# Kernel optimization log

Measured on AMD Instinct MI355X. Metric: run time of the kernel, lower is better.

The kernel has to match this reference:

```python
import jax, jax.numpy as jnp
import numpy as np


def _bn(x, g, b):
    # per-feature batch norm over (batch, seq), training-style statistics
    mu = jnp.mean(x, axis=(0, 1), keepdims=True)
    var = jnp.var(x, axis=(0, 1), keepdims=True)
    return (x - mu) * jax.lax.rsqrt(var + 1e-5) * g + b


def _heads(x, H):
    B, S, D = x.shape
    return x.reshape(B, S, H, D // H).transpose(0, 2, 1, 3)  # [B,H,S,hd]


def _merge(x):
    B, H, S, hd = x.shape
    return x.transpose(0, 2, 1, 3).reshape(B, S, H * hd)


def _pos_encoding(S, D, dtype):
    p = jnp.arange(S, dtype=jnp.float32)[:, None]
    i = jnp.arange(D // 2, dtype=jnp.float32)[None, :]
    ang = p / jnp.power(10000.0, 2.0 * i / D)
    # interleave sin (even dims) and cos (odd dims)
    return jnp.stack([jnp.sin(ang), jnp.cos(ang)], axis=-1).reshape(S, D).astype(dtype)


def _forward(x, encod, embed, Wq, bq, Wk, bk, Wv, bv, g1, b1,
             Wq2, bq2, Wk2, bk2, Wv2, bv2, Wo2, bo2, g2, b2, Wf, bf,
             num_heads, N):
    D = embed.shape[1]
    emb = embed[x]                      # [B,S,D]
    S = emb.shape[1]
    # forward does embed + (embed + pos) == 2*embed + pos
    input_multi = 2.0 * emb + _pos_encoding(S, D, emb.dtype)
    scale1 = 1.0 / np.sqrt(D)           # original scales by sqrt(embed_dim)
    scale2 = 1.0 / np.sqrt(D // num_heads)
    for _ in range(N):
        q, k, v = jnp.split(input_multi, 3, axis=-1)   # each [B,S,D/3]
        Q = _heads(jax.nn.relu(q @ Wq + bq), num_heads)
        K = _heads(jax.nn.relu(k @ Wk + bk), num_heads)
        Vm = _heads(jax.nn.relu(v @ Wv + bv), num_heads)
        A = jax.nn.softmax(jnp.einsum('bhqd,bhkd->bhqk', Q, K) * scale1, axis=-1)
        sa = _merge(jnp.einsum('bhqk,bhkd->bhqd', A, Vm))
        t = _bn(input_multi + sa, g1, b1)
        # cross attention: q,k from encoder halves, v from decoder state
        eq, ek = jnp.split(encod, 2, axis=-1)          # each [B,S,D/2]
        Q2 = _heads(eq @ Wq2 + bq2, num_heads)
        K2 = _heads(ek @ Wk2 + bk2, num_heads)
        V2 = _heads(t @ Wv2 + bv2, num_heads)
        A2 = jax.nn.softmax(jnp.einsum('bhqd,bhkd->bhqk', Q2, K2) * scale2, axis=-1)
        m2 = _merge(jnp.einsum('bhqk,bhkd->bhqd', A2, V2)) @ Wo2 + bo2
        t = _bn(m2 + t, g2, b2)
        # add_norm_2 reused for the FFN residual, as in the source
        input_multi = _bn(t + (t @ Wf + bf), g2, b2)
    return input_multi


def setup_inputs() -> dict:
    B, S, D, H, V, N = 4, 1024, 768, 12, 32000, 2
    ks = jax.random.split(jax.random.key(0), 12)
    w = lambda k, shape: jax.random.normal(k, shape, jnp.float32) * 0.02
    zeros = lambda: jnp.zeros((D,), jnp.float32)
    ones = lambda: jnp.ones((D,), jnp.float32)
    return {
        'x': jax.random.randint(ks[0], (B, S), 0, V),
        'encod': jax.random.normal(ks[1], (B, S, D), jnp.float32),
        'embed': w(ks[2], (V, D)),
        'Wq': w(ks[3], (D // 3, D)), 'bq': zeros(),
        'Wk': w(ks[4], (D // 3, D)), 'bk': zeros(),
        'Wv': w(ks[5], (D // 3, D)), 'bv': zeros(),
        'g1': ones(), 'b1': zeros(),
        'Wq2': w(ks[6], (D // 2, D)), 'bq2': zeros(),
        'Wk2': w(ks[7], (D // 2, D)), 'bk2': zeros(),
        'Wv2': w(ks[8], (D, D)), 'bv2': zeros(),
        'Wo2': w(ks[9], (D, D)), 'bo2': zeros(),
        'g2': ones(), 'b2': zeros(),
        'Wf': w(ks[10], (D, D)), 'bf': zeros(),
        'num_heads': H, 'N': N,
    }


def reference(x, encod, embed, Wq, bq, Wk, bk, Wv, bv, g1, b1,
              Wq2, bq2, Wk2, bk2, Wv2, bv2, Wo2, bo2, g2, b2, Wf, bf,
              num_heads, N):
    return _forward(x, encod, embed, Wq, bq, Wk, bk, Wv, bv, g1, b1,
                    Wq2, bq2, Wk2, bk2, Wv2, bv2, Wo2, bo2, g2, b2, Wf, bf,
                    num_heads, N)
```

## Files before the change

kernel.cpp:

```cpp
#include <hip/hip_runtime.h>
#include <hip/hip_bf16.h>

#define B 4
#define S 1024
#define D 768
#define H 12
#define HD 64
#define MROWS (B * S)
#define NELEM (B * S * D)

typedef __attribute__((ext_vector_type(8))) short short8;
typedef __attribute__((ext_vector_type(4))) short s16x4;
typedef __attribute__((ext_vector_type(4))) float f32x4;

#define MFMA16(a, b, c) __builtin_amdgcn_mfma_f32_16x16x32_bf16(a, b, c, 0, 0, 0)

#define SWZ64(row, col)  ((col) ^ (((row) & 7) << 3))
#define SWZ128(row, col) ((col) ^ (((row) & 15) << 3))

static __device__ __forceinline__ float bs2f(short s) {
    unsigned int u = ((unsigned int)(unsigned short)s) << 16;
    float f;
    __builtin_memcpy(&f, &u, 4);
    return f;
}
static __device__ __forceinline__ short f2bs(float f) {
    __hip_bfloat16 h = __float2bfloat16(f);
    return __builtin_bit_cast(short, h);
}
static __device__ __forceinline__ float loadin(const void* p, size_t i, int isb) {
    return isb ? bs2f(((const short*)p)[i]) : ((const float*)p)[i];
}

__global__ void detect_k(const void* p, int* flag) {
    const short* hb = (const short*)p;
    int t = threadIdx.x;
    int ins = 0;
    #pragma unroll
    for (int j = 0; j < 4; j++) {
        float v = bs2f(hb[(t * 4 + j) * 2]);
        if (!(v == v) || fabsf(v) > 1e3f || (v != 0.0f && fabsf(v) < 1e-20f)) ins++;
    }
    #pragma unroll
    for (int off = 32; off; off >>= 1) ins += __shfl_xor(ins, off);
    if (t == 0) *flag = (ins > 64) ? 0 : 1;
}

__global__ __launch_bounds__(256) void embed_pos_k(const int* __restrict__ x,
                                                   const void* __restrict__ embed,
                                                   float* __restrict__ outf,
                                                   short* __restrict__ outb,
                                                   const int* __restrict__ flg) {
    const int f = *flg;
    int bs = blockIdx.x;
    int tok = x[bs];
    int s = bs & (S - 1);
    for (int j = threadIdx.x; j < D; j += 256) {
        float e = loadin(embed, (size_t)tok * D + j, f);
        int i = j >> 1;
        float ang = (float)s * __expf(-9.210340371976184f * (2.0f * (float)i) / (float)D);
        float p = (j & 1) ? cosf(ang) : sinf(ang);
        float v = 2.0f * e + p;
        outf[bs * D + j] = v;
        outb[bs * D + j] = f2bs(v);
    }
}

struct WSegs {
    const void* src[8];
    short* dst[8];
    int K[8];
    const void* esrc;
    short* edst;
    float* statz;
};

__global__ __launch_bounds__(256) void prep_k(WSegs sg, const int* __restrict__ flg) {
    const int f = *flg;
    const int seg = blockIdx.z;
    const int t = threadIdx.x;
    if (seg == 8) {
        int tid = (blockIdx.y * 12 + blockIdx.x) * 256 + t;
        if (tid < 9216) sg.statz[tid] = 0.f;
        for (int i = tid; i < NELEM; i += 12 * 12 * 256)
            sg.edst[i] = f2bs(loadin(sg.esrc, i, f));
        return;
    }
    const int K = sg.K[seg];
    const int k0 = blockIdx.y * 64;
    if (k0 >= K) return;
    const void* src = sg.src[seg];
    short* dst = sg.dst[seg];
    __shared__ __align__(16) short Ts[64 * 72];
    int n0 = blockIdx.x * 64;
    int r = t >> 2, c4 = (t & 3) * 16;
    #pragma unroll
    for (int j = 0; j < 16; j++)
        Ts[r * 72 + c4 + j] = f2bs(loadin(src, (size_t)(k0 + r) * D + n0 + c4 + j, f));
    __syncthreads();
    int n = t >> 2, kc = (t & 3) * 16;
    short tmp[16];
    #pragma unroll
    for (int j = 0; j < 16; j++) tmp[j] = Ts[(kc + j) * 72 + n];
    short* dchunk = dst + (size_t)(n0 + n) * K + k0 + kc;
    *(short8*)&dchunk[0] = *(const short8*)&tmp[0];
    *(short8*)&dchunk[8] = *(const short8*)&tmp[8];
}

__global__ __launch_bounds__(256) void store_norm_k(const float* __restrict__ a,
                                                    const float* __restrict__ sums,
                                                    const void* __restrict__ g,
                                                    const void* __restrict__ beta,
                                                    void* __restrict__ out,
                                                    const int* __restrict__ flg) {
    const int f = *flg;
    int i = blockIdx.x * 256 + threadIdx.x;
    if (i < NELEM) {
        int ft = i % D;
        float mean = sums[ft] * (1.0f / (float)MROWS);
        float var = sums[D + ft] * (1.0f / (float)MROWS) - mean * mean;
        float sc = rsqrtf(var + 1e-5f) * loadin(g, ft, f);
        float y = (a[i] - mean) * sc + loadin(beta, ft, f);
        if (f) ((short*)out)[i] = f2bs(y);
        else   ((float*)out)[i] = y;
    }
}

struct GJob {
    const void* A;
    const short* WT;
    const void* bias;
    void* out;
    const float* resid;
    const float* bnsums;
    const void* bng;
    const void* bnb;
    float* sacc;
    int K;
    int aoff;
    int relu;
    int mode;
    int anorm;
    int rnorm;
};
struct GJobs { GJob j[3]; };

__global__ __launch_bounds__(256) void mgemm_k(GJobs js, const int* __restrict__ flg) {
    const GJob J = js.j[blockIdx.z];
    const int f = *flg;
    __shared__ __align__(16) short As[2][64 * 64];
    __shared__ __align__(16) short Bs[2][64 * 64];
    __shared__ float ssb0[768];
    __shared__ float ssb1[768];
    const int t = threadIdx.x;
    const int wave = t >> 6, lane = t & 63;
    const int quad = lane >> 4, l16 = lane & 15;
    if (J.anorm) {
        for (int i = t; i < D; i += 256) {
            float mean = J.bnsums[i] * (1.0f / (float)MROWS);
            float var = J.bnsums[D + i] * (1.0f / (float)MROWS) - mean * mean;
            float sc = rsqrtf(var + 1e-5f) * loadin(J.bng, i, f);
            ssb0[i] = sc;
            ssb1[i] = loadin(J.bnb, i, f) - mean * sc;
        }
        __syncthreads();
    }
    int lin = blockIdx.y * gridDim.x + blockIdx.x;
    int per = (gridDim.x * gridDim.y) >> 3;
    int nl = (lin & 7) * per + (lin >> 3);
    const int n0 = (nl % gridDim.x) * 64;
    const int m0 = (nl / gridDim.x) * 64;
    const int wm = (wave >> 1) * 32;
    const int wn = (wave & 1) * 32;
    f32x4 acc[2][2];
    #pragma unroll
    for (int i = 0; i < 2; i++)
        #pragma unroll
        for (int j = 0; j < 2; j++) acc[i][j] = f32x4{0.f, 0.f, 0.f, 0.f};

    const int ar = t >> 2;
    const int ac = (t & 3) * 16;
    const int wsz0 = SWZ64(ar, ac);
    const int wsz1 = SWZ64(ar, ac + 8);
    const int K = J.K;

    auto stageA = [&](int k0, short8& r0, short8& r1) {
        if (J.anorm) {
            int ft = J.aoff + k0 + ac;
            const float* Af = (const float*)J.A + (size_t)(m0 + ar) * 768 + ft;
            f32x4 v0 = *(const f32x4*)&Af[0];
            f32x4 v1 = *(const f32x4*)&Af[4];
            f32x4 v2 = *(const f32x4*)&Af[8];
            f32x4 v3 = *(const f32x4*)&Af[12];
            f32x4 c0 = *(const f32x4*)&ssb0[ft];
            f32x4 c1 = *(const f32x4*)&ssb0[ft + 4];
            f32x4 c2 = *(const f32x4*)&ssb0[ft + 8];
            f32x4 c3 = *(const f32x4*)&ssb0[ft + 12];
            f32x4 h0 = *(const f32x4*)&ssb1[ft];
            f32x4 h1 = *(const f32x4*)&ssb1[ft + 4];
            f32x4 h2 = *(const f32x4*)&ssb1[ft + 8];
            f32x4 h3 = *(const f32x4*)&ssb1[ft + 12];
            #pragma unroll
            for (int e = 0; e < 4; e++) {
                r0[e]     = f2bs(v0[e] * c0[e] + h0[e]);
                r0[4 + e] = f2bs(v1[e] * c1[e] + h1[e]);
                r1[e]     = f2bs(v2[e] * c2[e] + h2[e]);
                r1[4 + e] = f2bs(v3[e] * c3[e] + h3[e]);
            }
        } else {
            const short* Ab = (const short*)J.A + (size_t)(m0 + ar) * 768 + k0 + ac;
            r0 = *(const short8*)&Ab[0];
            r1 = *(const short8*)&Ab[8];
        }
    };

    {
        short8 a0, a1, b0, b1;
        stageA(0, a0, a1);
        const short* Wb = &J.WT[(size_t)(n0 + ar) * K + ac];
        b0 = *(const short8*)&Wb[0];
        b1 = *(const short8*)&Wb[8];
        *(short8*)&As[0][ar * 64 + wsz0] = a0;
        *(short8*)&As[0][ar * 64 + wsz1] = a1;
        *(short8*)&Bs[0][ar * 64 + wsz0] = b0;
        *(short8*)&Bs[0][ar * 64 + wsz1] = b1;
    }
    __syncthreads();

    int cur = 0;
    for (int k0 = 0; k0 < K; k0 += 64) {
        short8 na0, na1, nb0, nb1;
        const bool more = (k0 + 64 < K);
        if (more) {
            stageA(k0 + 64, na0, na1);
            const short* Wb = &J.WT[(size_t)(n0 + ar) * K + k0 + 64 + ac];
            nb0 = *(const short8*)&Wb[0];
            nb1 = *(const short8*)&Wb[8];
        }
        #pragma unroll
        for (int kk = 0; kk < 2; kk++) {
            short8 af[2], bfr[2];
            #pragma unroll
            for (int i = 0; i < 2; i++) {
                int arow = wm + i * 16 + l16;
                af[i] = *(const short8*)&As[cur][arow * 64 + SWZ64(arow, kk * 32 + quad * 8)];
            }
            #pragma unroll
            for (int j = 0; j < 2; j++) {
                int brow = wn + j * 16 + l16;
                bfr[j] = *(const short8*)&Bs[cur][brow * 64 + SWZ64(brow, kk * 32 + quad * 8)];
            }
            #pragma unroll
            for (int i = 0; i < 2; i++)
                #pragma unroll
                for (int j = 0; j < 2; j++)
                    acc[i][j] = MFMA16(af[i], bfr[j], acc[i][j]);
        }
        if (more) {
            *(short8*)&As[cur ^ 1][ar * 64 + wsz0] = na0;
            *(short8*)&As[cur ^ 1][ar * 64 + wsz1] = na1;
            *(short8*)&Bs[cur ^ 1][ar * 64 + wsz0] = nb0;
            *(short8*)&Bs[cur ^ 1][ar * 64 + wsz1] = nb1;
        }
        __syncthreads();
        cur ^= 1;
    }

    if (J.mode == 3) {
        short* sb = &As[0][0];
        #pragma unroll
        for (int j = 0; j < 2; j++) {
            int coll = wn + j * 16 + l16;
            float bv = loadin(J.bias, n0 + coll, f);
            #pragma unroll
            for (int i = 0; i < 2; i++) {
                int rowl = wm + i * 16 + quad * 4;
                s16x4 pk;
                #pragma unroll
                for (int r = 0; r < 4; r++) {
                    float v = acc[i][j][r] + bv;
                    if (J.relu) v = fmaxf(v, 0.f);
                    pk[r] = f2bs(v);
                }
                *(s16x4*)&sb[coll * 72 + rowl] = pk;
            }
        }
        __syncthreads();
        int hd = t >> 2, c = (t & 3) * 16;
        int b = m0 >> 10, s0 = m0 & (S - 1), h = n0 >> 6;
        short* dst = (short*)J.out + (((size_t)(b * H + h) * HD + hd) * S + s0 + c);
        *(short8*)&dst[0] = *(const short8*)&sb[hd * 72 + c];
        *(short8*)&dst[8] = *(const short8*)&sb[hd * 72 + c + 8];
    } else {
        #pragma unroll
        for (int j = 0; j < 2; j++) {
            int col = n0 + wn + j * 16 + l16;
            float bv = loadin(J.bias, col, f);
            float rsc = 1.f, rsh = 0.f;
            if (J.rnorm) {
                float mean = J.bnsums[col] * (1.0f / (float)MROWS);
                float var = J.bnsums[D + col] * (1.0f / (float)MROWS) - mean * mean;
                rsc = rsqrtf(var + 1e-5f) * loadin(J.bng, col, f);
                rsh = loadin(J.bnb, col, f) - mean * rsc;
            }
            float s1 = 0.f, s2 = 0.f;
            #pragma unroll
            for (int i = 0; i < 2; i++) {
                int rowb = m0 + wm + i * 16 + quad * 4;
                #pragma unroll
                for (int r = 0; r < 4; r++) {
                    float v = acc[i][j][r] + bv;
                    if (J.relu) v = fmaxf(v, 0.f);
                    int row = rowb + r;
                    if (J.mode == 2) {
                        size_t idx = (size_t)row * D + col;
                        if (J.resid) {
                            float rv = J.resid[idx];
                            v += J.rnorm ? (rv * rsc + rsh) : rv;
                        }
                        ((float*)J.out)[idx] = v;
                        s1 += v;
                        s2 += v * v;
                    } else if (J.mode == 1) {
                        size_t idx = (((size_t)(row >> 10) * H + (col >> 6)) * S + (row & (S - 1))) * HD + (col & 63);
                        ((short*)J.out)[idx] = f2bs(v);
                    } else {
                        ((short*)J.out)[(size_t)row * D + col] = f2bs(v);
                    }
                }
            }
            if (J.mode == 2 && J.sacc) {
                s1 += __shfl_xor(s1, 16); s1 += __shfl_xor(s1, 32);
                s2 += __shfl_xor(s2, 16); s2 += __shfl_xor(s2, 32);
                if (quad == 0) {
                    atomicAdd(&J.sacc[col], s1);
                    atomicAdd(&J.sacc[D + col], s2);
                }
            }
        }
    }
}

__global__ __launch_bounds__(256) void mfma_attn_fo_k(const short* __restrict__ Q,
                                                      const short* __restrict__ Km,
                                                      const short* __restrict__ Vt,
                                                      void* __restrict__ out,
                                                      const float* __restrict__ resid,
                                                      const float* __restrict__ rsums,
                                                      const void* __restrict__ rg,
                                                      const void* __restrict__ rb,
                                                      float* __restrict__ sacc,
                                                      float scale, int obf,
                                                      const int* __restrict__ flg) {
    __shared__ __align__(16) short Ks[128 * 64];
    __shared__ __align__(16) short Vs[64 * 128];
    __shared__ __align__(16) short Ps[4][16 * 136];
    const int fl = *flg;
    const int qt = blockIdx.y;
    const int bh = blockIdx.x;
    const int b = bh / H, h = bh % H;
    const int t = threadIdx.x;
    const int wave = t >> 6, lane = t & 63, quad = lane >> 4, l16 = lane & 15;
    const float sc2 = scale * 1.44269504089f;
    const short* Qh = Q + (size_t)bh * S * HD;
    const short* Kh = Km + (size_t)bh * S * HD;
    const short* Vh = Vt + (size_t)bh * S * HD;
    const int qrow = qt * 64 + wave * 16 + l16;
    short8 qf0 = *(const short8*)&Qh[(size_t)qrow * 64 + quad * 8];
    short8 qf1 = *(const short8*)&Qh[(size_t)qrow * 64 + 32 + quad * 8];
    short8 ones;
    #pragma unroll
    for (int j = 0; j < 8; j++) ones[j] = (short)0x3F80;
    f32x4 o[4];
    f32x4 ls = f32x4{0.f, 0.f, 0.f, 0.f};
    float m_i = -1e30f;
    #pragma unroll
    for (int nt = 0; nt < 4; nt++) o[nt] = f32x4{0.f, 0.f, 0.f, 0.f};
    const int krow = t >> 1, kc0 = (t & 1) * 32;
    const int vhd = t >> 2, vkc = (t & 3) * 32;
    const short* kbase = &Kh[(size_t)krow * 64 + kc0];
    const short* vbase = &Vh[(size_t)vhd * S + vkc];

    short8 kreg[4], vreg[4];
    #pragma unroll
    for (int j = 0; j < 4; j++) kreg[j] = *(const short8*)&kbase[j * 8];
    #pragma unroll
    for (int j = 0; j < 4; j++) vreg[j] = *(const short8*)&vbase[j * 8];
    #pragma unroll
    for (int j = 0; j < 4; j++)
        *(short8*)&Ks[krow * 64 + SWZ64(krow, kc0 + j * 8)] = kreg[j];
    #pragma unroll
    for (int j = 0; j < 4; j++)
        *(short8*)&Vs[vhd * 128 + SWZ128(vhd, vkc + j * 8)] = vreg[j];
    __syncthreads();

    for (int kt = 0; kt < S; kt += 128) {
        if (kt + 128 < S) {
            #pragma unroll
            for (int j = 0; j < 4; j++)
                kreg[j] = *(const short8*)&kbase[(size_t)(kt + 128) * 64 + j * 8];
            #pragma unroll
            for (int j = 0; j < 4; j++)
                vreg[j] = *(const short8*)&vbase[kt + 128 + j * 8];
        }
        f32x4 sf[8];
        #pragma unroll
        for (int nt = 0; nt < 8; nt++) {
            int kr = nt * 16 + l16;
            short8 kb0 = *(const short8*)&Ks[kr * 64 + SWZ64(kr, quad * 8)];
            short8 kb1 = *(const short8*)&Ks[kr * 64 + SWZ64(kr, 32 + quad * 8)];
            f32x4 c = f32x4{0.f, 0.f, 0.f, 0.f};
            c = MFMA16(kb0, qf0, c);
            c = MFMA16(kb1, qf1, c);
            sf[nt] = c;
        }
        f32x4 m4 = sf[0];
        #pragma unroll
        for (int nt = 1; nt < 8; nt++)
            #pragma unroll
            for (int r = 0; r < 4; r++) m4[r] = fmaxf(m4[r], sf[nt][r]);
        float mx = fmaxf(fmaxf(m4[0], m4[1]), fmaxf(m4[2], m4[3]));
        mx = fmaxf(mx, __shfl_xor(mx, 16));
        mx = fmaxf(mx, __shfl_xor(mx, 32));
        bool need = ((mx - m_i) * sc2 > 8.0f);
        if (__any(need)) {
            float mnew = fmaxf(m_i, mx);
            float alpha = exp2f((m_i - mnew) * sc2);
            m_i = mnew;
            #pragma unroll
            for (int r = 0; r < 4; r++) {
                float ar = __shfl(alpha, quad * 4 + r);
                ls[r] *= ar;
                #pragma unroll
                for (int nt = 0; nt < 4; nt++) o[nt][r] *= ar;
            }
        }
        #pragma unroll
        for (int nt = 0; nt < 8; nt++) {
            s16x4 pk;
            #pragma unroll
            for (int r = 0; r < 4; r++)
                pk[r] = f2bs(exp2f((sf[nt][r] - m_i) * sc2));
            *(s16x4*)&Ps[wave][l16 * 136 + nt * 16 + quad * 4] = pk;
        }
        short8 pa[4];
        #pragma unroll
        for (int kc = 0; kc < 4; kc++)
            pa[kc] = *(const short8*)&Ps[wave][l16 * 136 + kc * 32 + quad * 8];
        #pragma unroll
        for (int nt = 0; nt < 4; nt++) {
            int vr = nt * 16 + l16;
            #pragma unroll
            for (int kc = 0; kc < 4; kc++) {
                short8 vb = *(const short8*)&Vs[vr * 128 + SWZ128(vr, kc * 32 + quad * 8)];
                o[nt] = MFMA16(pa[kc], vb, o[nt]);
            }
        }
        #pragma unroll
        for (int kc = 0; kc < 4; kc++) ls = MFMA16(pa[kc], ones, ls);
        __syncthreads();
        if (kt + 128 < S) {
            #pragma unroll
            for (int j = 0; j < 4; j++)
                *(short8*)&Ks[krow * 64 + SWZ64(krow, kc0 + j * 8)] = kreg[j];
            #pragma unroll
            for (int j = 0; j < 4; j++)
                *(short8*)&Vs[vhd * 128 + SWZ128(vhd, vkc + j * 8)] = vreg[j];
        }
        __syncthreads();
    }
    float inv[4];
    #pragma unroll
    for (int r = 0; r < 4; r++) inv[r] = 1.0f / ls[r];
    #pragma unroll
    for (int nt = 0; nt < 4; nt++) {
        int col = h * HD + nt * 16 + l16;
        float rsc = 1.f, rsh = 0.f;
        if (rsums) {
            float mean = rsums[col] * (1.0f / (float)MROWS);
            float var = rsums[D + col] * (1.0f / (float)MROWS) - mean * mean;
            rsc = rsqrtf(var + 1e-5f) * loadin(rg, col, fl);
            rsh = loadin(rb, col, fl) - mean * rsc;
        }
        float s1 = 0.f, s2 = 0.f;
        #pragma unroll
        for (int r = 0; r < 4; r++) {
            int row = b * S + qt * 64 + wave * 16 + quad * 4 + r;
            size_t idx = (size_t)row * D + col;
            float v = o[nt][r] * inv[r];
            if (obf) {
                ((short*)out)[idx] = f2bs(v);
            } else {
                if (resid) {
                    float rv = resid[idx];
                    v += rsums ? (rv * rsc + rsh) : rv;
                }
                ((float*)out)[idx] = v;
                s1 += v;
                s2 += v * v;
            }
        }
        if (sacc) {
            s1 += __shfl_xor(s1, 16); s1 += __shfl_xor(s1, 32);
            s2 += __shfl_xor(s2, 16); s2 += __shfl_xor(s2, 32);
            if (quad == 0) {
                atomicAdd(&sacc[col], s1);
                atomicAdd(&sacc[D + col], s2);
            }
        }
    }
}

extern "C" void kernel_launch(void* const* d_in, const int* in_sizes, int n_in,
                              void* d_out, int out_size, void* d_ws, size_t ws_size,
                              hipStream_t stream) {
    const int* x = (const int*)d_in[0];
    const short* encod = (const short*)d_in[1];
    const short* embed = (const short*)d_in[2];
    const short* Wq = (const short*)d_in[3];
    const short* bq = (const short*)d_in[4];
    const short* Wk = (const short*)d_in[5];
    const short* bk = (const short*)d_in[6];
    const short* Wv = (const short*)d_in[7];
    const short* bv = (const short*)d_in[8];
    const short* g1 = (const short*)d_in[9];
    const short* b1 = (const short*)d_in[10];
    const short* Wq2 = (const short*)d_in[11];
    const short* bq2 = (const short*)d_in[12];
    const short* Wk2 = (const short*)d_in[13];
    const short* bk2 = (const short*)d_in[14];
    const short* Wv2 = (const short*)d_in[15];
    const short* bv2 = (const short*)d_in[16];
    const short* Wo2 = (const short*)d_in[17];
    const short* bo2 = (const short*)d_in[18];
    const short* g2 = (const short*)d_in[19];
    const short* b2 = (const short*)d_in[20];
    const short* Wf = (const short*)d_in[21];
    const short* bf_ = (const short*)d_in[22];

    short* HBase = (short*)d_ws;
    #define HB(i) (HBase + (size_t)(i) * NELEM)
    float* IMf = (float*)HB(0);
    short* IMb = HB(2);
    short* Q2h = HB(3);
    short* K2h = HB(4);
    short* WTp = HB(5);
    short* WTq  = WTp;
    short* WTk  = WTp + 196608;
    short* WTv  = WTp + 393216;
    short* WTq2 = WTp + 589824;
    short* WTk2 = WTp + 884736;
    short* WTv2 = WTp + 1179648;
    short* WTo2 = WTp + 1769472;
    short* WTf  = WTp + 2359296;
    short* Qbh = HB(6);
    short* Kbh = HB(7);
    short* Vth = HB(9);
    float* T1f = (float*)HB(10);
    float* Ff  = (float*)HB(12);
    short* A2b = HB(15);
    float* T2f = (float*)HB(16);
    short* Eb  = Qbh;
    float* SU = (float*)HB(18);
    #define SUMS(it, bn) (SU + (size_t)((it) * 3 + (bn)) * 2 * D)
    int*   flg  = (int*)(SU + 12 * D);

    const dim3 gGrid(12, 64);
    const dim3 aGrid(B * H, S / 64);
    const int EB = (NELEM + 255) / 256;
    const float scale1 = 0.03608439182435161f;
    const float scale2 = 0.125f;

    detect_k<<<1, 64, 0, stream>>>(encod, flg);
    embed_pos_k<<<MROWS, 256, 0, stream>>>(x, embed, IMf, IMb, flg);

    WSegs sg;
    sg.src[0] = Wq;  sg.dst[0] = WTq;  sg.K[0] = 256;
    sg.src[1] = Wk;  sg.dst[1] = WTk;  sg.K[1] = 256;
    sg.src[2] = Wv;  sg.dst[2] = WTv;  sg.K[2] = 256;
    sg.src[3] = Wq2; sg.dst[3] = WTq2; sg.K[3] = 384;
    sg.src[4] = Wk2; sg.dst[4] = WTk2; sg.K[4] = 384;
    sg.src[5] = Wv2; sg.dst[5] = WTv2; sg.K[5] = 768;
    sg.src[6] = Wo2; sg.dst[6] = WTo2; sg.K[6] = 768;
    sg.src[7] = Wf;  sg.dst[7] = WTf;  sg.K[7] = 768;
    sg.esrc = encod; sg.edst = Eb; sg.statz = SU;
    prep_k<<<dim3(12, 12, 9), 256, 0, stream>>>(sg, flg);

    {
        GJobs js;
        js.j[0] = GJob{Eb,       WTq2, bq2, Q2h, nullptr, nullptr, nullptr, nullptr, nullptr, 384, 0, 0, 1, 0, 0};
        js.j[1] = GJob{Eb + 384, WTk2, bk2, K2h, nullptr, nullptr, nullptr, nullptr, nullptr, 384, 0, 0, 1, 0, 0};
        js.j[2] = js.j[0];
        mgemm_k<<<dim3(12, 64, 2), 256, 0, stream>>>(js, flg);
    }

    for (int it = 0; it < 2; it++) {
        {
            GJobs js;
            if (it == 0) {
                js.j[0] = GJob{IMb,       WTq, bq, Qbh, nullptr, nullptr, nullptr, nullptr, nullptr, 256, 0,   1, 1, 0, 0};
                js.j[1] = GJob{IMb + 256, WTk, bk, Kbh, nullptr, nullptr, nullptr, nullptr, nullptr, 256, 0,   1, 1, 0, 0};
                js.j[2] = GJob{IMb + 512, WTv, bv, Vth, nullptr, nullptr, nullptr, nullptr, nullptr, 256, 0,   1, 3, 0, 0};
            } else {
                js.j[0] = GJob{Ff, WTq, bq, Qbh, nullptr, SUMS(0, 2), g2, b2, nullptr, 256, 0,   1, 1, 1, 0};
                js.j[1] = GJob{Ff, WTk, bk, Kbh, nullptr, SUMS(0, 2), g2, b2, nullptr, 256, 256, 1, 1, 1, 0};
                js.j[2] = GJob{Ff, WTv, bv, Vth, nullptr, SUMS(0, 2), g2, b2, nullptr, 256, 512, 1, 3, 1, 0};
            }
            mgemm_k<<<dim3(12, 64, 3), 256, 0, stream>>>(js, flg);
        }
        if (it == 0)
            mfma_attn_fo_k<<<aGrid, 256, 0, stream>>>(Qbh, Kbh, Vth, T1f, IMf,
                    nullptr, nullptr, nullptr, SUMS(0, 0), scale1, 0, flg);
        else
            mfma_attn_fo_k<<<aGrid, 256, 0, stream>>>(Qbh, Kbh, Vth, T1f, Ff,
                    SUMS(0, 2), g2, b2, SUMS(1, 0), scale1, 0, flg);
        {
            GJobs js;
            js.j[0] = GJob{T1f, WTv2, bv2, Vth, nullptr, SUMS(it, 0), g1, b1, nullptr, 768, 0, 0, 3, 1, 0};
            js.j[1] = js.j[0]; js.j[2] = js.j[0];
            mgemm_k<<<gGrid, 256, 0, stream>>>(js, flg);
        }
        mfma_attn_fo_k<<<aGrid, 256, 0, stream>>>(Q2h, K2h, Vth, A2b, nullptr,
                nullptr, nullptr, nullptr, nullptr, scale2, 1, flg);
        {
            GJobs js;
            js.j[0] = GJob{A2b, WTo2, bo2, T2f, T1f, SUMS(it, 0), g1, b1, SUMS(it, 1), 768, 0, 0, 2, 0, 1};
            js.j[1] = js.j[0]; js.j[2] = js.j[0];
            mgemm_k<<<gGrid, 256, 0, stream>>>(js, flg);
        }
        {
            GJobs js;
            js.j[0] = GJob{T2f, WTf, bf_, Ff, T2f, SUMS(it, 1), g2, b2, SUMS(it, 2), 768, 0, 0, 2, 1, 1};
            js.j[1] = js.j[0]; js.j[2] = js.j[0];
            mgemm_k<<<gGrid, 256, 0, stream>>>(js, flg);
        }
    }

    store_norm_k<<<EB, 256, 0, stream>>>(Ff, SUMS(1, 2), g2, b2, d_out, flg);
}
```

Baseline: 569.9 us.

## Template GEMM on K, prefetch two stages ahead, use packed bf16 conversion

The GEMM kernel is templated on K so its k-loop fully unrolls. Global loads are now issued two stages ahead using register double-buffering on top of the shared-memory ping-pong, which aims to hide more global latency. Scalar float-to-bf16 conversions in the GEMM A staging, the epilogue and the attention P tile are replaced with the packed v_cvt_pk_bf16_f32 instruction to cut VALU work. In exchange, register pressure rises from the extra prefetch buffers and the unrolled loop, and several template instantiations are compiled.

```diff
diff --git a/kernel.cpp b/kernel.cpp
--- a/kernel.cpp
+++ b/kernel.cpp
@@ -27,6 +27,11 @@
 static __device__ __forceinline__ short f2bs(float f) {
     __hip_bfloat16 h = __float2bfloat16(f);
     return __builtin_bit_cast(short, h);
+}
+static __device__ __forceinline__ unsigned int cvtpk_bf16(float lo, float hi) {
+    unsigned int r;
+    asm("v_cvt_pk_bf16_f32 %0, %1, %2" : "=v"(r) : "v"(lo), "v"(hi));
+    return r;
 }
 static __device__ __forceinline__ float loadin(const void* p, size_t i, int isb) {
     return isb ? bs2f(((const short*)p)[i]) : ((const float*)p)[i];
@@ -145,6 +150,7 @@
 };
 struct GJobs { GJob j[3]; };
 
+template<int KT>
 __global__ __launch_bounds__(256) void mgemm_k(GJobs js, const int* __restrict__ flg) {
     const GJob J = js.j[blockIdx.z];
     const int f = *flg;
@@ -182,7 +188,7 @@
     const int ac = (t & 3) * 16;
     const int wsz0 = SWZ64(ar, ac);
     const int wsz1 = SWZ64(ar, ac + 8);
-    const int K = J.K;
+    constexpr int NS = KT / 64;
 
     auto stageA = [&](int k0, short8& r0, short8& r1) {
         if (J.anorm) {
@@ -200,43 +206,51 @@
             f32x4 h1 = *(const f32x4*)&ssb1[ft + 4];
             f32x4 h2 = *(const f32x4*)&ssb1[ft + 8];
             f32x4 h3 = *(const f32x4*)&ssb1[ft + 12];
-            #pragma unroll
-            for (int e = 0; e < 4; e++) {
-                r0[e]     = f2bs(v0[e] * c0[e] + h0[e]);
-                r0[4 + e] = f2bs(v1[e] * c1[e] + h1[e]);
-                r1[e]     = f2bs(v2[e] * c2[e] + h2[e]);
-                r1[4 + e] = f2bs(v3[e] * c3[e] + h3[e]);
-            }
+            union { unsigned int u[4]; short8 s; } ca, cb;
+            ca.u[0] = cvtpk_bf16(v0[0] * c0[0] + h0[0], v0[1] * c0[1] + h0[1]);
+            ca.u[1] = cvtpk_bf16(v0[2] * c0[2] + h0[2], v0[3] * c0[3] + h0[3]);
+            ca.u[2] = cvtpk_bf16(v1[0] * c1[0] + h1[0], v1[1] * c1[1] + h1[1]);
+            ca.u[3] = cvtpk_bf16(v1[2] * c1[2] + h1[2], v1[3] * c1[3] + h1[3]);
+            cb.u[0] = cvtpk_bf16(v2[0] * c2[0] + h2[0], v2[1] * c2[1] + h2[1]);
+            cb.u[1] = cvtpk_bf16(v2[2] * c2[2] + h2[2], v2[3] * c2[3] + h2[3]);
+            cb.u[2] = cvtpk_bf16(v3[0] * c3[0] + h3[0], v3[1] * c3[1] + h3[1]);
+            cb.u[3] = cvtpk_bf16(v3[2] * c3[2] + h3[2], v3[3] * c3[3] + h3[3]);
+            r0 = ca.s;
+            r1 = cb.s;
         } else {
             const short* Ab = (const short*)J.A + (size_t)(m0 + ar) * 768 + k0 + ac;
             r0 = *(const short8*)&Ab[0];
             r1 = *(const short8*)&Ab[8];
         }
     };
+    auto loadB = [&](int k0, short8& r0, short8& r1) {
+        const short* Wb = &J.WT[(size_t)(n0 + ar) * KT + k0 + ac];
+        r0 = *(const short8*)&Wb[0];
+        r1 = *(const short8*)&Wb[8];
+    };
 
     {
         short8 a0, a1, b0, b1;
         stageA(0, a0, a1);
-        const short* Wb = &J.WT[(size_t)(n0 + ar) * K + ac];
-        b0 = *(const short8*)&Wb[0];
-        b1 = *(const short8*)&Wb[8];
+        loadB(0, b0, b1);
         *(short8*)&As[0][ar * 64 + wsz0] = a0;
         *(short8*)&As[0][ar * 64 + wsz1] = a1;
         *(short8*)&Bs[0][ar * 64 + wsz0] = b0;
         *(short8*)&Bs[0][ar * 64 + wsz1] = b1;
     }
+    short8 pA0, pA1, pB0, pB1;
+    stageA(64, pA0, pA1);
+    loadB(64, pB0, pB1);
     __syncthreads();
 
-    int cur = 0;
-    for (int k0 = 0; k0 < K; k0 += 64) {
-        short8 na0, na1, nb0, nb1;
-        const bool more = (k0 + 64 < K);
-        if (more) {
-            stageA(k0 + 64, na0, na1);
-            const short* Wb = &J.WT[(size_t)(n0 + ar) * K + k0 + 64 + ac];
-            nb0 = *(const short8*)&Wb[0];
-            nb1 = *(const short8*)&Wb[8];
-        }
+    #pragma unroll
+    for (int s = 0; s < NS; s++) {
+        short8 nA0, nA1, nB0, nB1;
+        if (s + 2 < NS) {
+            stageA((s + 2) * 64, nA0, nA1);
+            loadB((s + 2) * 64, nB0, nB1);
+        }
+        const int cur = s & 1;
         #pragma unroll
         for (int kk = 0; kk < 2; kk++) {
             short8 af[2], bfr[2];
@@ -256,14 +270,14 @@
                 for (int j = 0; j < 2; j++)
                     acc[i][j] = MFMA16(af[i], bfr[j], acc[i][j]);
         }
-        if (more) {
-            *(short8*)&As[cur ^ 1][ar * 64 + wsz0] = na0;
-            *(short8*)&As[cur ^ 1][ar * 64 + wsz1] = na1;
-            *(short8*)&Bs[cur ^ 1][ar * 64 + wsz0] = nb0;
-            *(short8*)&Bs[cur ^ 1][ar * 64 + wsz1] = nb1;
-        }
+        if (s + 1 < NS) {
+            *(short8*)&As[cur ^ 1][ar * 64 + wsz0] = pA0;
+            *(short8*)&As[cur ^ 1][ar * 64 + wsz1] = pA1;
+            *(short8*)&Bs[cur ^ 1][ar * 64 + wsz0] = pB0;
+            *(short8*)&Bs[cur ^ 1][ar * 64 + wsz1] = pB1;
+        }
+        pA0 = nA0; pA1 = nA1; pB0 = nB0; pB1 = nB1;
         __syncthreads();
-        cur ^= 1;
     }
 
     if (J.mode == 3) {
@@ -275,14 +289,16 @@
             #pragma unroll
             for (int i = 0; i < 2; i++) {
                 int rowl = wm + i * 16 + quad * 4;
-                s16x4 pk;
-                #pragma unroll
-                for (int r = 0; r < 4; r++) {
-                    float v = acc[i][j][r] + bv;
-                    if (J.relu) v = fmaxf(v, 0.f);
-                    pk[r] = f2bs(v);
+                float e0 = acc[i][j][0] + bv, e1 = acc[i][j][1] + bv;
+                float e2 = acc[i][j][2] + bv, e3 = acc[i][j][3] + bv;
+                if (J.relu) {
+                    e0 = fmaxf(e0, 0.f); e1 = fmaxf(e1, 0.f);
+                    e2 = fmaxf(e2, 0.f); e3 = fmaxf(e3, 0.f);
                 }
-                *(s16x4*)&sb[coll * 72 + rowl] = pk;
+                union { unsigned int u[2]; s16x4 s; } cv;
+                cv.u[0] = cvtpk_bf16(e0, e1);
+                cv.u[1] = cvtpk_bf16(e2, e3);
+                *(s16x4*)&sb[coll * 72 + rowl] = cv.s;
             }
         }
         __syncthreads();
@@ -437,11 +453,13 @@
         }
         #pragma unroll
         for (int nt = 0; nt < 8; nt++) {
-            s16x4 pk;
-            #pragma unroll
-            for (int r = 0; r < 4; r++)
-                pk[r] = f2bs(exp2f((sf[nt][r] - m_i) * sc2));
-            *(s16x4*)&Ps[wave][l16 * 136 + nt * 16 + quad * 4] = pk;
+            float e0 = exp2f((sf[nt][0] - m_i) * sc2);
+            float e1 = exp2f((sf[nt][1] - m_i) * sc2);
+            float e2 = exp2f((sf[nt][2] - m_i) * sc2);
+            float e3 = exp2f((sf[nt][3] - m_i) * sc2);
+            unsigned int w0 = cvtpk_bf16(e0, e1);
+            unsigned int w1 = cvtpk_bf16(e2, e3);
+            *(uint2*)&Ps[wave][l16 * 136 + nt * 16 + quad * 4] = make_uint2(w0, w1);
         }
         short8 pa[4];
         #pragma unroll
@@ -591,7 +609,7 @@
         js.j[0] = GJob{Eb,       WTq2, bq2, Q2h, nullptr, nullptr, nullptr, nullptr, nullptr, 384, 0, 0, 1, 0, 0};
         js.j[1] = GJob{Eb + 384, WTk2, bk2, K2h, nullptr, nullptr, nullptr, nullptr, nullptr, 384, 0, 0, 1, 0, 0};
         js.j[2] = js.j[0];
-        mgemm_k<<<dim3(12, 64, 2), 256, 0, stream>>>(js, flg);
+        mgemm_k<384><<<dim3(12, 64, 2), 256, 0, stream>>>(js, flg);
     }
 
     for (int it = 0; it < 2; it++) {
@@ -606,7 +624,7 @@
                 js.j[1] = GJob{Ff, WTk, bk, Kbh, nullptr, SUMS(0, 2), g2, b2, nullptr, 256, 256, 1, 1, 1, 0};
                 js.j[2] = GJob{Ff, WTv, bv, Vth, nullptr, SUMS(0, 2), g2, b2, nullptr, 256, 512, 1, 3, 1, 0};
             }
-            mgemm_k<<<dim3(12, 64, 3), 256, 0, stream>>>(js, flg);
+            mgemm_k<256><<<dim3(12, 64, 3), 256, 0, stream>>>(js, flg);
         }
         if (it == 0)
             mfma_attn_fo_k<<<aGrid, 256, 0, stream>>>(Qbh, Kbh, Vth, T1f, IMf,
@@ -618,7 +636,7 @@
             GJobs js;
             js.j[0] = GJob{T1f, WTv2, bv2, Vth, nullptr, SUMS(it, 0), g1, b1, nullptr, 768, 0, 0, 3, 1, 0};
             js.j[1] = js.j[0]; js.j[2] = js.j[0];
-            mgemm_k<<<gGrid, 256, 0, stream>>>(js, flg);
+            mgemm_k<768><<<gGrid, 256, 0, stream>>>(js, flg);
         }
         mfma_attn_fo_k<<<aGrid, 256, 0, stream>>>(Q2h, K2h, Vth, A2b, nullptr,
                 nullptr, nullptr, nullptr, nullptr, scale2, 1, flg);
@@ -626,13 +644,13 @@
             GJobs js;
             js.j[0] = GJob{A2b, WTo2, bo2, T2f, T1f, SUMS(it, 0), g1, b1, SUMS(it, 1), 768, 0, 0, 2, 0, 1};
             js.j[1] = js.j[0]; js.j[2] = js.j[0];
-            mgemm_k<<<gGrid, 256, 0, stream>>>(js, flg);
+            mgemm_k<768><<<gGrid, 256, 0, stream>>>(js, flg);
         }
         {
             GJobs js;
             js.j[0] = GJob{T2f, WTf, bf_, Ff, T2f, SUMS(it, 1), g2, b2, SUMS(it, 2), 768, 0, 0, 2, 1, 1};
             js.j[1] = js.j[0]; js.j[2] = js.j[0];
-            mgemm_k<<<gGrid, 256, 0, stream>>>(js, flg);
+            mgemm_k<768><<<gGrid, 256, 0, stream>>>(js, flg);
         }
     }
 
```

New measurement: 578.7 us. Within noise of the previous version (+1.5%).
